# Performance work log

Hardware: AMD Instinct MI355X
Metric: run time of the kernel (lower is better)

Reference implementation:

```python
import jax, jax.numpy as jnp
import numpy as np

NUM_CLASSES = 20
K = 3
STRIDE = 32
IMG = 2048


def setup_inputs() -> dict:
    key = jax.random.key(0)
    k1, k2, k3, k4, k5, k6, k7 = jax.random.split(key, 7)
    B, Cin, H, W = 2, 1024, 64, 64
    N = 1000
    feats = jax.random.normal(k1, (B, Cin, H, W), jnp.float32)
    s = 1.0 / np.sqrt(Cin).astype(np.float32)
    w_cls = jax.random.normal(k2, ((NUM_CLASSES + 1) * K * K, Cin), jnp.float32) * s
    b_cls = jax.random.normal(k3, ((NUM_CLASSES + 1) * K * K,), jnp.float32) * 0.01
    w_reg = jax.random.normal(k4, (4 * K * K, Cin), jnp.float32) * s
    b_reg = jax.random.normal(k5, (4 * K * K,), jnp.float32) * 0.01
    # proposals in image pixel coords (x1, y1, x2, y2), guaranteed non-empty
    xy1 = jax.random.randint(k6, (B, N, 2), 0, IMG - 64)
    wh = jax.random.randint(k7, (B, N, 2), STRIDE, 512)
    xy2 = jnp.minimum(xy1 + wh, IMG)
    proposals = jnp.concatenate([xy1, xy2], axis=-1).astype(jnp.int32)
    return {"features": feats, "w_cls": w_cls, "b_cls": b_cls,
            "w_reg": w_reg, "b_reg": b_reg, "proposals": proposals}


def _psroi(scores, proposals, groups):
    """Faithful to the source: adaptive_avg_pool2d bin (0,0) per channel,
    then sum over the K*K channel groups (stride-::K*K indexing in torch)."""
    B, C, H, W = scores.shape
    N = proposals.shape[1]
    p = proposals.astype(jnp.float32) / STRIDE
    x1 = jnp.floor(p[..., 0]).astype(jnp.int32)  # [B,N]
    y1 = jnp.floor(p[..., 1]).astype(jnp.int32)
    x2 = jnp.ceil(p[..., 2]).astype(jnp.int32)
    y2 = jnp.ceil(p[..., 3]).astype(jnp.int32)
    # adaptive_avg_pool2d bin (0,0): rows [0, ceil(h/K)), cols [0, ceil(w/K)) of the crop
    hb = (y2 - y1 + K - 1) // K
    wb = (x2 - x1 + K - 1) // K
    r = jnp.arange(H)
    c = jnp.arange(W)
    rmask = (r[None, None, :] >= y1[..., None]) & (r[None, None, :] < (y1 + hb)[..., None])  # [B,N,H]
    cmask = (c[None, None, :] >= x1[..., None]) & (c[None, None, :] < (x1 + wb)[..., None])  # [B,N,W]
    mask = (rmask[..., :, None] & cmask[..., None, :]).astype(scores.dtype)  # [B,N,H,W]
    denom = (hb * wb).astype(scores.dtype)
    pooled = jnp.einsum('bohw,bnhw->bno', scores, mask) / denom[..., None]  # bin(0,0) avg, all channels
    # channel index = cls_group * K*K + g ; torch ::K*K picks (g, spatial_bin 0) then sums over g
    return pooled.reshape(B, N, groups, K * K).sum(-1)


def reference(features, w_cls, b_cls, w_reg, b_reg, proposals):
    cls_scores = jnp.einsum('bchw,oc->bohw', features, w_cls) + b_cls[None, :, None, None]
    reg_scores = jnp.einsum('bchw,oc->bohw', features, w_reg) + b_reg[None, :, None, None]
    cls_out = _psroi(cls_scores, proposals, NUM_CLASSES + 1)  # [B,N,21]
    reg_out = _psroi(reg_scores, proposals, 4)                # [B,N,4]
    return (cls_out, reg_out)
```

## Files before the change

kernel.cpp:

```cpp
#include <hip/hip_runtime.h>


#define HW 4096
#define NG 25
#define CIN 1024
#define B 2
#define NPROP 1000
#define NCH 4
#define CK (CIN / NCH)
#define NSL 16
#define CS (CK / NSL)
#define MHW (B * NG * HW)

__global__ void rfcn_wfold(const float* __restrict__ w_cls,
                           const float* __restrict__ b_cls,
                           const float* __restrict__ w_reg,
                           const float* __restrict__ b_reg,
                           float* __restrict__ Wred,
                           float* __restrict__ Bred) {
    int i = blockIdx.x * 256 + threadIdx.x;
    if (i < NG * CIN) {
        int g = i >> 10, c = i & (CIN - 1);
        float s = 0.f;
        if (g < 21) {
            #pragma unroll
            for (int k = 0; k < 9; ++k) s += w_cls[(size_t)(g * 9 + k) * CIN + c];
        } else {
            int gr = g - 21;
            #pragma unroll
            for (int k = 0; k < 9; ++k) s += w_reg[(size_t)(gr * 9 + k) * CIN + c];
        }
        Wred[i] = s;
    } else if (i < NG * CIN + NG) {
        int g = i - NG * CIN;
        float s = 0.f;
        if (g < 21) {
            #pragma unroll
            for (int k = 0; k < 9; ++k) s += b_cls[g * 9 + k];
        } else {
            #pragma unroll
            for (int k = 0; k < 9; ++k) s += b_reg[(g - 21) * 9 + k];
        }
        Bred[g] = s;
    }
}

__global__ __launch_bounds__(1024, 8)
void rfcn_proj(const float* __restrict__ feats,
               const float* __restrict__ Wred,
               float* __restrict__ part) {
    const int t = threadIdx.x;
    const int p = t & 63;
    const int sl = __builtin_amdgcn_readfirstlane(t >> 6);
    const int pix0 = blockIdx.x * 64;
    const int chunk = blockIdx.y;
    const int b = blockIdx.z;
    const int c0 = chunk * CK + sl * CS;

    const float* __restrict__ f = feats + ((size_t)b * CIN + c0) * HW + pix0 + p;
    const float* __restrict__ wgt = Wred + c0;

    float acc[NG];
    #pragma unroll
    for (int g = 0; g < NG; ++g) acc[g] = 0.f;

    #pragma unroll
    for (int cc = 0; cc < CS; cc += 8) {
        float fv[8];
        #pragma unroll
        for (int j = 0; j < 8; ++j) fv[j] = f[(size_t)(cc + j) * HW];
        #pragma unroll
        for (int j = 0; j < 8; ++j)
            #pragma unroll
            for (int g = 0; g < NG; ++g)
                acc[g] += fv[j] * wgt[g * CIN + cc + j];
    }

    __shared__ float red[(NSL / 2) * NG * 64];
    if (sl >= 8) {
        #pragma unroll
        for (int g = 0; g < NG; ++g) red[((sl - 8) * NG + g) * 64 + p] = acc[g];
    }
    __syncthreads();
    if (sl < 8) {
        #pragma unroll
        for (int g = 0; g < NG; ++g) red[(sl * NG + g) * 64 + p] += acc[g];
    }
    __syncthreads();

    float* __restrict__ o = part + ((size_t)(chunk * B + b) * NG) * HW + pix0;
    for (int idx = t; idx < NG * 64; idx += 1024) {
        const int g = idx >> 6, pp = idx & 63;
        float s = 0.f;
        #pragma unroll
        for (int ss = 0; ss < NSL / 2; ++ss) s += red[(ss * NG + g) * 64 + pp];
        o[(size_t)g * HW + pp] = s;
    }
}

__global__ __launch_bounds__(1024)
void rfcn_integral_gather(const float* __restrict__ part,
                          const int* __restrict__ props,
                          const float* __restrict__ Bred,
                          float* __restrict__ out) {
    const int m = blockIdx.x;
    const int t = threadIdx.x;
    const int lane = t & 63;
    const int wave = t >> 6;
    const int b = m / NG;
    const int g = m - b * NG;
    __shared__ float tile[64 * 65];

    #pragma unroll
    for (int i = 0; i < 4; ++i) {
        const int idx = i * 1024 + t;
        float v[NCH];
        #pragma unroll
        for (int ch = 0; ch < NCH; ++ch)
            v[ch] = part[(size_t)(ch * (B * NG) + m) * HW + idx];
        #pragma unroll
        for (int off = NCH / 2; off >= 1; off >>= 1)
            #pragma unroll
            for (int j = 0; j < off; ++j) v[j] += v[j + off];
        tile[(idx >> 6) * 65 + (idx & 63)] = v[0];
    }
    __syncthreads();

    #pragma unroll
    for (int i = 0; i < 4; ++i) {
        const int row = wave * 4 + i;
        float v = tile[row * 65 + lane];
        #pragma unroll
        for (int d = 1; d < 64; d <<= 1) {
            float u = __shfl_up(v, (unsigned)d, 64);
            if (lane >= d) v += u;
        }
        tile[row * 65 + lane] = v;
    }
    __syncthreads();

    #pragma unroll
    for (int i = 0; i < 4; ++i) {
        const int col = wave * 4 + i;
        float v = tile[lane * 65 + col];
        #pragma unroll
        for (int d = 1; d < 64; d <<= 1) {
            float u = __shfl_up(v, (unsigned)d, 64);
            if (lane >= d) v += u;
        }
        tile[lane * 65 + col] = v;
    }
    __syncthreads();

    const float bias = Bred[g];
    const int n = t;
    if (n < NPROP) {
        const int4 pr = ((const int4*)props)[b * NPROP + n];
        const int x1 = pr.x >> 5;
        const int y1 = pr.y >> 5;
        const int x2 = (pr.z + 31) >> 5;
        const int y2 = (pr.w + 31) >> 5;
        const int wb = (x2 - x1 + 2) / 3;
        const int hb = (y2 - y1 + 2) / 3;
        const int c2 = x1 + wb - 1;
        const int r2 = y1 + hb - 1;

        float s = tile[r2 * 65 + c2];
        if (x1 > 0)           s -= tile[r2 * 65 + (x1 - 1)];
        if (y1 > 0)           s -= tile[(y1 - 1) * 65 + c2];
        if (x1 > 0 && y1 > 0) s += tile[(y1 - 1) * 65 + (x1 - 1)];
        const float v = bias + s / (float)(hb * wb);
        if (g < 21)
            out[(size_t)(b * NPROP + n) * 21 + g] = v;
        else
            out[(size_t)(B * NPROP * 21) + (size_t)(b * NPROP + n) * 4 + (g - 21)] = v;
    }
}

extern "C" void kernel_launch(void* const* d_in, const int* in_sizes, int n_in,
                              void* d_out, int out_size, void* d_ws, size_t ws_size,
                              hipStream_t stream) {
    const float* feats = (const float*)d_in[0];
    const float* w_cls = (const float*)d_in[1];
    const float* b_cls = (const float*)d_in[2];
    const float* w_reg = (const float*)d_in[3];
    const float* b_reg = (const float*)d_in[4];
    const int*   props = (const int*)d_in[5];
    float* out = (float*)d_out;
    float* ws  = (float*)d_ws;

    float* Wred = ws;
    float* Bred = ws + 25600;
    float* part = ws + 25632;

    rfcn_wfold<<<(NG * CIN + NG + 255) / 256, 256, 0, stream>>>(
        w_cls, b_cls, w_reg, b_reg, Wred, Bred);
    rfcn_proj<<<dim3(HW / 64, NCH, B), 1024, 0, stream>>>(feats, Wred, part);
    rfcn_integral_gather<<<B * NG, 1024, 0, stream>>>(part, props, Bred, out);
}
```

Measured before the change: 28.36 us.

## Stage feature tiles into LDS via direct global-to-LDS loads, widen pixel tile

```diff
diff --git a/kernel.cpp b/kernel.cpp
--- a/kernel.cpp
+++ b/kernel.cpp
@@ -8,9 +8,14 @@
 #define NPROP 1000
 #define NCH 4
 #define CK (CIN / NCH)
-#define NSL 16
-#define CS (CK / NSL)
+#define PX 128
 #define MHW (B * NG * HW)
+
+__device__ __forceinline__ void gload_lds16(const float* g, float* l) {
+    __builtin_amdgcn_global_load_lds(
+        (const __attribute__((address_space(1))) void*)g,
+        (__attribute__((address_space(3))) void*)l, 16, 0, 0);
+}
 
 __global__ void rfcn_wfold(const float* __restrict__ w_cls,
                            const float* __restrict__ b_cls,
@@ -45,56 +50,69 @@
     }
 }
 
-__global__ __launch_bounds__(1024, 8)
+__global__ __launch_bounds__(1024)
 void rfcn_proj(const float* __restrict__ feats,
                const float* __restrict__ Wred,
                float* __restrict__ part) {
     const int t = threadIdx.x;
-    const int p = t & 63;
-    const int sl = __builtin_amdgcn_readfirstlane(t >> 6);
-    const int pix0 = blockIdx.x * 64;
+    const int lane = t & 63;
+    const int wv = __builtin_amdgcn_readfirstlane(t >> 6);
+    const int pix0 = blockIdx.x * PX;
     const int chunk = blockIdx.y;
     const int b = blockIdx.z;
-    const int c0 = chunk * CK + sl * CS;
-
-    const float* __restrict__ f = feats + ((size_t)b * CIN + c0) * HW + pix0 + p;
-    const float* __restrict__ wgt = Wred + c0;
+
+    __shared__ float smem[CK * PX];
+
+    const float* fbase = feats + ((size_t)b * CIN + chunk * CK) * HW + pix0;
+    #pragma unroll
+    for (int i = 0; i < 8; ++i) {
+        const int seg = wv * 8 + i;
+        const float* g = fbase + (size_t)(2 * seg + (lane >> 5)) * HW
+                       + (lane & 31) * 4;
+        gload_lds16(g, smem + seg * 256);
+    }
+    asm volatile("s_waitcnt vmcnt(0)" ::: "memory");
+    __syncthreads();
+
+    const int s = wv >> 1;
+    const int q = wv & 1;
+    const int p = q * 64 + lane;
+    const float* __restrict__ wgt = Wred + chunk * CK + s * 32;
 
     float acc[NG];
     #pragma unroll
     for (int g = 0; g < NG; ++g) acc[g] = 0.f;
 
     #pragma unroll
-    for (int cc = 0; cc < CS; cc += 8) {
+    for (int cc = 0; cc < 32; cc += 8) {
         float fv[8];
         #pragma unroll
-        for (int j = 0; j < 8; ++j) fv[j] = f[(size_t)(cc + j) * HW];
+        for (int j = 0; j < 8; ++j)
+            fv[j] = smem[(s * 32 + cc + j) * PX + p];
         #pragma unroll
         for (int j = 0; j < 8; ++j)
             #pragma unroll
             for (int g = 0; g < NG; ++g)
                 acc[g] += fv[j] * wgt[g * CIN + cc + j];
     }
-
-    __shared__ float red[(NSL / 2) * NG * 64];
-    if (sl >= 8) {
-        #pragma unroll
-        for (int g = 0; g < NG; ++g) red[((sl - 8) * NG + g) * 64 + p] = acc[g];
-    }
-    __syncthreads();
-    if (sl < 8) {
-        #pragma unroll
-        for (int g = 0; g < NG; ++g) red[(sl * NG + g) * 64 + p] += acc[g];
-    }
-    __syncthreads();
-
-    float* __restrict__ o = part + ((size_t)(chunk * B + b) * NG) * HW + pix0;
-    for (int idx = t; idx < NG * 64; idx += 1024) {
-        const int g = idx >> 6, pp = idx & 63;
-        float s = 0.f;
-        #pragma unroll
-        for (int ss = 0; ss < NSL / 2; ++ss) s += red[(ss * NG + g) * 64 + pp];
-        o[(size_t)g * HW + pp] = s;
+    __syncthreads();
+
+    float* red = smem;
+    if (s > 0) {
+        #pragma unroll
+        for (int g = 0; g < NG; ++g) red[((s - 1) * NG + g) * PX + p] = acc[g];
+    }
+    __syncthreads();
+    if (s == 0) {
+        float* __restrict__ o =
+            part + ((size_t)(chunk * B + b) * NG) * HW + pix0;
+        #pragma unroll
+        for (int g = 0; g < NG; ++g) {
+            float v = acc[g];
+            #pragma unroll
+            for (int k = 0; k < 7; ++k) v += red[(k * NG + g) * PX + p];
+            o[(size_t)g * HW + p] = v;
+        }
     }
 }
 
@@ -195,6 +213,6 @@
 
     rfcn_wfold<<<(NG * CIN + NG + 255) / 256, 256, 0, stream>>>(
         w_cls, b_cls, w_reg, b_reg, Wred, Bred);
-    rfcn_proj<<<dim3(HW / 64, NCH, B), 1024, 0, stream>>>(feats, Wred, part);
+    rfcn_proj<<<dim3(HW / PX, NCH, B), 1024, 0, stream>>>(feats, Wred, part);
     rfcn_integral_gather<<<B * NG, 1024, 0, stream>>>(part, props, Bred, out);
 }
```

Measured after the change: 31.46 us. +10.9%, slower.
